# Kernel optimization log

Measured on AMD Instinct MI355X. Metric: run time of the kernel, lower is better.

The kernel has to match this reference:

```python
import jax, jax.numpy as jnp
import numpy as np

N_FLOWS = 40
S, D = 2048, 16384  # samples, latent dim n*q (n=8192, q=2)


def setup_inputs() -> dict:
    key = jax.random.key(0)
    kx, kw, ku, kb = jax.random.split(key, 4)
    X = jax.random.normal(kx, (S, D), dtype=jnp.float32)
    # Learned planar-flow parameters, stacked over the 40 layers.
    ws = jax.random.normal(kw, (N_FLOWS, D), dtype=jnp.float32) * 0.01
    us = jax.random.normal(ku, (N_FLOWS, D), dtype=jnp.float32) * 0.01
    bs = jax.random.normal(kb, (N_FLOWS,), dtype=jnp.float32) * 0.01
    return {"X": X, "ws": ws, "us": us, "bs": bs}


def _planar_chain(X, ws, us, bs):
    def step(x, params):
        w, u, b = params  # w,u: [D], b: scalar
        wu = jnp.dot(w, u)
        # invertibility constraint: m(a) = -1 + softplus(a)
        u_hat = u + ((-1.0 + jax.nn.softplus(wu)) - wu) * w / jnp.dot(w, w)
        act = jnp.tanh(x @ w + b)            # [S]
        return x + act[:, None] * u_hat, None  # rank-1 update

    X, _ = jax.lax.scan(step, X, (ws, us, bs))
    return X


def reference(X, ws, us, bs):
    return _planar_chain(X, ws, us, bs)
```

## Files before the change

### kernel.cpp

```cpp
#include <hip/hip_runtime.h>
#include <math.h>

#define D      16384
#define D4     4096
#define S      2048
#define NF     40
#define NFP    48
#define ROWS   8
#define TPB    1024
#define CH4    256
#define CHUNK  1024
#define NCHUNK 16
#define KSPLIT 8

#define WW_OFF     0
#define UW_OFF     1600
#define COEF_OFF   3200
#define AT_OFF     4096
#define WB_OFF     (AT_OFF + NF * S)
#define C0P_OFF    (WB_OFF + (NFP * D) / 2)
#define WS_NEED    (C0P_OFF + S * KSPLIT * NF)

typedef __attribute__((ext_vector_type(8))) __bf16 bf16x8;
typedef __attribute__((ext_vector_type(4))) float  f32x4;
union FragU { unsigned u[4]; bf16x8 b; };

__device__ __forceinline__ float dot4(float4 a, float4 b) {
    return fmaf(a.x, b.x, fmaf(a.y, b.y, fmaf(a.z, b.z, a.w * b.w)));
}
__device__ __forceinline__ void fma4(float4& o, float a, float4 u) {
    o.x = fmaf(a, u.x, o.x); o.y = fmaf(a, u.y, o.y);
    o.z = fmaf(a, u.z, o.z); o.w = fmaf(a, u.w, o.w);
}
__device__ __forceinline__ unsigned bpack(float lo, float hi) {
    unsigned a = __float_as_uint(lo);
    unsigned b = __float_as_uint(hi);
    a += 0x7fffu + ((a >> 16) & 1u);
    b += 0x7fffu + ((b >> 16) & 1u);
    return (a >> 16) | (b & 0xffff0000u);
}

__global__ __launch_bounds__(512) void pair_wb_kernel(const float* __restrict__ Wg,
                                                      const float* __restrict__ Ug,
                                                      float* __restrict__ tbl) {
    const int k = blockIdx.x >> 3;
    const int h = blockIdx.x & 7;
    const int t = threadIdx.x;
    uint2* Wb2 = (uint2*)((unsigned*)(tbl + WB_OFF) + (size_t)k * (D / 2));

    if (k >= NF) {
        Wb2[h * 512 + t] = make_uint2(0u, 0u);
        return;
    }

    const int j0 = h * 5;
    const int wave = t >> 6, lane = t & 63;
    const float4* W4 = (const float4*)Wg;
    const float4* U4 = (const float4*)Ug;

    float ww[5], wu[5], wkk = 0.f, wku = 0.f;
    float4 wkSave;
    #pragma unroll
    for (int j = 0; j < 5; ++j) { ww[j] = 0.f; wu[j] = 0.f; }

    for (int i = 0; i < 8; ++i) {
        const int pos = i * 512 + t;
        float4 wk = W4[(size_t)k * D4 + pos];
        float4 uk = U4[(size_t)k * D4 + pos];
        if (i == h) wkSave = wk;
        wkk += dot4(wk, wk);
        wku += dot4(wk, uk);
        #pragma unroll
        for (int j = 0; j < 5; ++j) {
            float4 wj = W4[(size_t)(j0 + j) * D4 + pos];
            float4 uj = U4[(size_t)(j0 + j) * D4 + pos];
            ww[j] += dot4(wk, wj);
            wu[j] += dot4(wk, uj);
        }
    }

    {
        uint2 p;
        p.x = bpack(wkSave.x, wkSave.y);
        p.y = bpack(wkSave.z, wkSave.w);
        Wb2[h * 512 + t] = p;
    }

    float v[12];
    #pragma unroll
    for (int j = 0; j < 5; ++j) { v[j] = ww[j]; v[5 + j] = wu[j]; }
    v[10] = wkk; v[11] = wku;
    #pragma unroll
    for (int e = 0; e < 12; ++e) {
        #pragma unroll
        for (int off = 32; off >= 1; off >>= 1) v[e] += __shfl_xor(v[e], off);
    }

    __shared__ float red[8][12];
    __shared__ float fin[12];
    if (lane == 0) {
        #pragma unroll
        for (int e = 0; e < 12; ++e) red[wave][e] = v[e];
    }
    __syncthreads();
    if (t < 12) {
        float s = 0.f;
        #pragma unroll
        for (int w = 0; w < 8; ++w) s += red[w][t];
        fin[t] = s;
        if (t < 5)       tbl[WW_OFF + k * NF + j0 + t] = s;
        else if (t < 10) tbl[UW_OFF + k * NF + j0 + (t - 5)] = s;
    }
    __syncthreads();
    if (t == 0 && h == 0) {
        float wwd = fin[10], wud = fin[11];
        float sp = (wud > 0.f) ? (wud + log1pf(expf(-wud))) : log1pf(expf(wud));
        tbl[COEF_OFF + k] = ((-1.f + sp) - wud) / wwd;
    }
}

__global__ __launch_bounds__(256) void gemm_part_kernel(const float* __restrict__ Xg,
                                                        float* __restrict__ tbl) {
    const int t = threadIdx.x, w = t >> 6, l = t & 63;
    const int rt = blockIdx.x >> 3, ks = blockIdx.x & 7;
    const int r = l & 15, kg = l >> 4;

    __shared__ float red[4][16][NFP + 1];

    const unsigned* WbU = (const unsigned*)(tbl + WB_OFF);
    f32x4 acc0 = {0.f, 0.f, 0.f, 0.f};
    f32x4 acc1 = acc0, acc2 = acc0;

    const float*    xrow = Xg + (size_t)(rt * 16 + r) * D + kg * 8;
    const unsigned* b0p = WbU + (size_t)(r)      * (D / 2) + kg * 4;
    const unsigned* b1p = WbU + (size_t)(16 + r) * (D / 2) + kg * 4;
    const unsigned* b2p = WbU + (size_t)(32 + r) * (D / 2) + kg * 4;
    const int kbase = ks * 2048 + w * 512;

    #pragma unroll 4
    for (int kk = 0; kk < 512; kk += 32) {
        const int kb = kbase + kk;
        float4 xa = *(const float4*)(xrow + kb);
        float4 xb = *(const float4*)(xrow + kb + 4);
        FragU af;
        af.u[0] = bpack(xa.x, xa.y); af.u[1] = bpack(xa.z, xa.w);
        af.u[2] = bpack(xb.x, xb.y); af.u[3] = bpack(xb.z, xb.w);
        const int ku = kb >> 1;
        bf16x8 b0 = *(const bf16x8*)(b0p + ku);
        bf16x8 b1 = *(const bf16x8*)(b1p + ku);
        bf16x8 b2 = *(const bf16x8*)(b2p + ku);
        acc0 = __builtin_amdgcn_mfma_f32_16x16x32_bf16(af.b, b0, acc0, 0, 0, 0);
        acc1 = __builtin_amdgcn_mfma_f32_16x16x32_bf16(af.b, b1, acc1, 0, 0, 0);
        acc2 = __builtin_amdgcn_mfma_f32_16x16x32_bf16(af.b, b2, acc2, 0, 0, 0);
    }

    #pragma unroll
    for (int q = 0; q < 4; ++q) {
        red[w][kg * 4 + q][r]      = acc0[q];
        red[w][kg * 4 + q][16 + r] = acc1[q];
        red[w][kg * 4 + q][32 + r] = acc2[q];
    }
    __syncthreads();

    float* c0p = tbl + C0P_OFF;
    for (int e = t; e < 16 * NF; e += 256) {
        const int row = e / NF, fl = e - row * NF;
        float s = red[0][row][fl] + red[1][row][fl] +
                  red[2][row][fl] + red[3][row][fl];
        c0p[((size_t)(rt * 16 + row) * KSPLIT + ks) * NF + fl] = s;
    }
}

__global__ __launch_bounds__(1024) void reduce_rec_kernel(const float* __restrict__ Bg,
                                                          float* __restrict__ tbl) {
    const int t = threadIdx.x;
    const int wave = t >> 6, lane = t & 63;

    __shared__ float gts[NF][NF + 1];
    __shared__ float bsS[NF];
    for (int e = t; e < NF * NF; e += 1024) {
        const int jj = e % NF;
        gts[e / NF][jj] = tbl[UW_OFF + e] + tbl[COEF_OFF + jj] * tbl[WW_OFF + e];
    }
    if (t < NF) bsS[t] = Bg[t];
    __syncthreads();

    const int g = blockIdx.x * 16 + wave;
    const float* cp = tbl + C0P_OFF + (size_t)g * (KSPLIT * NF);

    float c0 = 0.f;
    if (lane < NF) {
        #pragma unroll
        for (int s = 0; s < KSPLIT; ++s) c0 += cp[s * NF + lane];
        c0 += bsS[lane];
    }

    float aj = 0.f;
    for (int k = 0; k < NF; ++k) {
        float gv = (lane < k) ? gts[k][lane] : 0.f;
        float tv = aj * gv;
        #pragma unroll
        for (int off = 32; off >= 1; off >>= 1) tv += __shfl_xor(tv, off);
        float ck = __shfl(c0, k);
        float ak = tanhf(ck + tv);
        if (lane == k) aj = ak;
    }
    if (lane < NF) tbl[AT_OFF + (size_t)lane * S + g] = aj;
}

__global__ __launch_bounds__(256) void apply_kernel(const float* __restrict__ Xg,
                                                    const float* __restrict__ Wg,
                                                    const float* __restrict__ Ug,
                                                    const float* __restrict__ tbl,
                                                    float* __restrict__ Og) {
    const int bid = blockIdx.x;
    const int rblk = bid >> 3, cq = bid & 7;
    const int t = threadIdx.x;
    const int r0 = rblk * 8;

    const float4* X4 = (const float4*)Xg;
    const float4* W4 = (const float4*)Wg;
    const float4* U4 = (const float4*)Ug;
    const float*  aT = tbl + AT_OFF;
    float4* O4 = (float4*)Og;

    #pragma unroll 1
    for (int p = 0; p < 2; ++p) {
        const int col = cq * 512 + p * 256 + t;
        float4 o[8];
        #pragma unroll
        for (int r = 0; r < 8; ++r)
            o[r] = X4[(size_t)(r0 + r) * D4 + col];

        #pragma unroll 2
        for (int k = 0; k < NF; ++k) {
            float4 wv = W4[(size_t)k * D4 + col];
            float4 uu = U4[(size_t)k * D4 + col];
            const float cf = tbl[COEF_OFF + k];
            float4 uh;
            uh.x = fmaf(cf, wv.x, uu.x);
            uh.y = fmaf(cf, wv.y, uu.y);
            uh.z = fmaf(cf, wv.z, uu.z);
            uh.w = fmaf(cf, wv.w, uu.w);
            const float* ap = aT + (size_t)k * S + r0;
            fma4(o[0], ap[0], uh); fma4(o[1], ap[1], uh);
            fma4(o[2], ap[2], uh); fma4(o[3], ap[3], uh);
            fma4(o[4], ap[4], uh); fma4(o[5], ap[5], uh);
            fma4(o[6], ap[6], uh); fma4(o[7], ap[7], uh);
        }
        #pragma unroll
        for (int r = 0; r < 8; ++r)
            O4[(size_t)(r0 + r) * D4 + col] = o[r];
    }
}

__global__ __launch_bounds__(TPB) void flow_main_fb(const float* __restrict__ Xg,
                                                    const float* __restrict__ Wg,
                                                    const float* __restrict__ Ug,
                                                    const float* __restrict__ Bg,
                                                    const float* __restrict__ tbl,
                                                    float* __restrict__ Og) {
    const int t = threadIdx.x;
    const int wave = t >> 6, lane = t & 63;
    const int rowBase = blockIdx.x * ROWS;

    __shared__ __align__(16) float xs[2][ROWS][CHUNK];
    __shared__ __align__(16) float gts[NF][NF + 1];
    __shared__ __align__(16) float c0p[NF][ROWS];
    __shared__ __align__(16) float aTs[NF][ROWS];
    __shared__ float bsS[NF];
    __shared__ float coefS[NF];

    const float4* X4 = (const float4*)Xg;
    const float4* W4 = (const float4*)Wg;
    const float4* U4 = (const float4*)Ug;

    for (int e = t; e < NF * NF; e += TPB) {
        const int jj = e % NF;
        gts[e / NF][jj] = tbl[UW_OFF + e] + tbl[COEF_OFF + jj] * tbl[WW_OFF + e];
    }
    if (t < NF) { bsS[t] = Bg[t]; coefS[t] = tbl[COEF_OFF + t]; }

    const int srow = (t >> 8) * 2;
    const int sc4  = t & 255;

    float4 p0 = X4[(size_t)(rowBase + srow)     * D4 + sc4];
    float4 p1 = X4[(size_t)(rowBase + srow + 1) * D4 + sc4];
    *(float4*)&xs[0][srow][sc4 * 4]     = p0;
    *(float4*)&xs[0][srow + 1][sc4 * 4] = p1;
    __syncthreads();

    const int kt = wave & 7, rt = wave >> 3;
    const int k0 = kt * 5, r0 = rt * 4;

    float acc[4][5];
    #pragma unroll
    for (int r = 0; r < 4; ++r)
        #pragma unroll
        for (int kk = 0; kk < 5; ++kk) acc[r][kk] = 0.f;

    int b = 0;
    for (int c = 0; c < NCHUNK; ++c) {
        if (c + 1 < NCHUNK) {
            p0 = X4[(size_t)(rowBase + srow)     * D4 + (c + 1) * CH4 + sc4];
            p1 = X4[(size_t)(rowBase + srow + 1) * D4 + (c + 1) * CH4 + sc4];
        }
        #pragma unroll 1
        for (int s = 0; s < 4; ++s) {
            const int col4 = c * CH4 + s * 64 + lane;
            float4 wv[5];
            #pragma unroll
            for (int kk = 0; kk < 5; ++kk)
                wv[kk] = W4[(size_t)(k0 + kk) * D4 + col4];
            const int lc = (s * 64 + lane) * 4;
            #pragma unroll
            for (int r = 0; r < 4; ++r) {
                float4 xv = *(const float4*)&xs[b][r0 + r][lc];
                #pragma unroll
                for (int kk = 0; kk < 5; ++kk)
                    acc[r][kk] = fmaf(xv.x, wv[kk].x,
                                 fmaf(xv.y, wv[kk].y,
                                 fmaf(xv.z, wv[kk].z,
                                 fmaf(xv.w, wv[kk].w, acc[r][kk]))));
            }
        }
        if (c + 1 < NCHUNK) {
            *(float4*)&xs[b ^ 1][srow][sc4 * 4]     = p0;
            *(float4*)&xs[b ^ 1][srow + 1][sc4 * 4] = p1;
        }
        __syncthreads();
        b ^= 1;
    }

    #pragma unroll
    for (int r = 0; r < 4; ++r)
        #pragma unroll
        for (int kk = 0; kk < 5; ++kk) {
            float v = acc[r][kk];
            #pragma unroll
            for (int off = 32; off >= 1; off >>= 1) v += __shfl_xor(v, off);
            acc[r][kk] = v;
        }
    if (lane == 0) {
        #pragma unroll
        for (int kk = 0; kk < 5; ++kk)
            #pragma unroll
            for (int r = 0; r < 4; ++r)
                c0p[k0 + kk][r0 + r] = acc[r][kk];
    }
    __syncthreads();

    float4 o[ROWS];
    {
        const int col = wave * 64 + lane;
        #pragma unroll
        for (int r = 0; r < ROWS; ++r)
            o[r] = X4[(size_t)(rowBase + r) * D4 + col];
    }

    if (wave < ROWS) {
        const int r = wave, j = lane;
        float aj = 0.f;
        for (int k = 0; k < NF; ++k) {
            float gv = (j < k) ? gts[k][j] : 0.f;
            float tv = aj * gv;
            #pragma unroll
            for (int off = 32; off >= 1; off >>= 1) tv += __shfl_xor(tv, off);
            float sum = c0p[k][r] + bsS[k] + tv;
            float ak = tanhf(sum);
            if (j == k) aj = ak;
        }
        if (j < NF) aTs[j][r] = aj;
    }
    __syncthreads();

    float4* O4 = (float4*)Og;
    #pragma unroll 1
    for (int p = 0; p < 4; ++p) {
        const int col = p * 1024 + wave * 64 + lane;
        if (p > 0) {
            #pragma unroll
            for (int r = 0; r < ROWS; ++r)
                o[r] = X4[(size_t)(rowBase + r) * D4 + col];
        }
        #pragma unroll 2
        for (int k = 0; k < NF; ++k) {
            float4 uu = U4[(size_t)k * D4 + col];
            float4 wv = W4[(size_t)k * D4 + col];
            const float cf = coefS[k];
            float4 uh;
            uh.x = fmaf(cf, wv.x, uu.x);
            uh.y = fmaf(cf, wv.y, uu.y);
            uh.z = fmaf(cf, wv.z, uu.z);
            uh.w = fmaf(cf, wv.w, uu.w);
            float4 alo = *(const float4*)&aTs[k][0];
            float4 ahi = *(const float4*)&aTs[k][4];
            fma4(o[0], alo.x, uh); fma4(o[1], alo.y, uh);
            fma4(o[2], alo.z, uh); fma4(o[3], alo.w, uh);
            fma4(o[4], ahi.x, uh); fma4(o[5], ahi.y, uh);
            fma4(o[6], ahi.z, uh); fma4(o[7], ahi.w, uh);
        }
        #pragma unroll
        for (int r = 0; r < ROWS; ++r)
            O4[(size_t)(rowBase + r) * D4 + col] = o[r];
    }
}

extern "C" void kernel_launch(void* const* d_in, const int* in_sizes, int n_in,
                              void* d_out, int out_size, void* d_ws, size_t ws_size,
                              hipStream_t stream) {
    const float* X  = (const float*)d_in[0];
    const float* Wg = (const float*)d_in[1];
    const float* Ug = (const float*)d_in[2];
    const float* Bg = (const float*)d_in[3];
    float* out = (float*)d_out;
    float* tbl = (float*)d_ws;

    const bool fast = ws_size >= (size_t)WS_NEED * sizeof(float);

    if (fast) {
        pair_wb_kernel<<<NFP * 8, 512, 0, stream>>>(Wg, Ug, tbl);
        gemm_part_kernel<<<(S / 16) * KSPLIT, 256, 0, stream>>>(X, tbl);
        reduce_rec_kernel<<<S / 16, 1024, 0, stream>>>(Bg, tbl);
        apply_kernel<<<(S / 8) * 8, 256, 0, stream>>>(X, Wg, Ug, tbl, out);
    } else {
        pair_wb_kernel<<<NF * 8, 512, 0, stream>>>(Wg, Ug, tbl);
        flow_main_fb<<<S / ROWS, TPB, 0, stream>>>(X, Wg, Ug, Bg, tbl, out);
    }
}
```

Baseline: 142.9 us.

## Precompute u_hat once and stage activations in LDS for apply kernel

Adds a small kernel that materializes u_hat = u + coef*w for all flows into workspace, so the apply kernel reads one vector per flow instead of two plus a coefficient. The activation table is transposed to row-major [S][NF], and each apply block loads its 8x40 slice into shared memory, reading it as float4 instead of scattered scalar global loads. This cuts per-block global traffic and scalar loads in the hot loop, at the cost of an extra launch and a u_hat write/read pass (about 2.6MB). The fallback path skips the bf16 W pack.

```diff
diff --git a/kernel.cpp b/kernel.cpp
--- a/kernel.cpp
+++ b/kernel.cpp
@@ -19,6 +19,7 @@
 #define AT_OFF     4096
 #define WB_OFF     (AT_OFF + NF * S)
 #define C0P_OFF    (WB_OFF + (NFP * D) / 2)
+#define UH_OFF     C0P_OFF
 #define WS_NEED    (C0P_OFF + S * KSPLIT * NF)
 
 typedef __attribute__((ext_vector_type(8))) __bf16 bf16x8;
@@ -42,7 +43,8 @@
 
 __global__ __launch_bounds__(512) void pair_wb_kernel(const float* __restrict__ Wg,
                                                       const float* __restrict__ Ug,
-                                                      float* __restrict__ tbl) {
+                                                      float* __restrict__ tbl,
+                                                      int doWb) {
     const int k = blockIdx.x >> 3;
     const int h = blockIdx.x & 7;
     const int t = threadIdx.x;
@@ -79,7 +81,7 @@
         }
     }
 
-    {
+    if (doWb) {
         uint2 p;
         p.x = bpack(wkSave.x, wkSave.y);
         p.y = bpack(wkSave.z, wkSave.w);
@@ -205,12 +207,25 @@
         float ak = tanhf(ck + tv);
         if (lane == k) aj = ak;
     }
-    if (lane < NF) tbl[AT_OFF + (size_t)lane * S + g] = aj;
+    if (lane < NF) tbl[AT_OFF + (size_t)g * NF + lane] = aj;
+}
+
+__global__ __launch_bounds__(256) void uh_kernel(const float* __restrict__ Wg,
+                                                 const float* __restrict__ Ug,
+                                                 float* __restrict__ tbl) {
+    const int k = blockIdx.x >> 4;
+    const int h = blockIdx.x & 15;
+    const float cf = tbl[COEF_OFF + k];
+    const int i = h * 256 + threadIdx.x;
+    const float4 w = ((const float4*)Wg)[(size_t)k * D4 + i];
+    const float4 u = ((const float4*)Ug)[(size_t)k * D4 + i];
+    float4 r;
+    r.x = fmaf(cf, w.x, u.x); r.y = fmaf(cf, w.y, u.y);
+    r.z = fmaf(cf, w.z, u.z); r.w = fmaf(cf, w.w, u.w);
+    ((float4*)(tbl + UH_OFF))[(size_t)k * D4 + i] = r;
 }
 
 __global__ __launch_bounds__(256) void apply_kernel(const float* __restrict__ Xg,
-                                                    const float* __restrict__ Wg,
-                                                    const float* __restrict__ Ug,
                                                     const float* __restrict__ tbl,
                                                     float* __restrict__ Og) {
     const int bid = blockIdx.x;
@@ -218,10 +233,15 @@
     const int t = threadIdx.x;
     const int r0 = rblk * 8;
 
-    const float4* X4 = (const float4*)Xg;
-    const float4* W4 = (const float4*)Wg;
-    const float4* U4 = (const float4*)Ug;
-    const float*  aT = tbl + AT_OFF;
+    __shared__ __align__(16) float aL[NF][8];
+    for (int e = t; e < NF * 8; e += 256) {
+        const int r = e / NF, k = e - r * NF;
+        aL[k][r] = tbl[AT_OFF + (size_t)(r0 + r) * NF + k];
+    }
+    __syncthreads();
+
+    const float4* X4  = (const float4*)Xg;
+    const float4* UH4 = (const float4*)(tbl + UH_OFF);
     float4* O4 = (float4*)Og;
 
     #pragma unroll 1
@@ -232,21 +252,15 @@
         for (int r = 0; r < 8; ++r)
             o[r] = X4[(size_t)(r0 + r) * D4 + col];
 
-        #pragma unroll 2
+        #pragma unroll 4
         for (int k = 0; k < NF; ++k) {
-            float4 wv = W4[(size_t)k * D4 + col];
-            float4 uu = U4[(size_t)k * D4 + col];
-            const float cf = tbl[COEF_OFF + k];
-            float4 uh;
-            uh.x = fmaf(cf, wv.x, uu.x);
-            uh.y = fmaf(cf, wv.y, uu.y);
-            uh.z = fmaf(cf, wv.z, uu.z);
-            uh.w = fmaf(cf, wv.w, uu.w);
-            const float* ap = aT + (size_t)k * S + r0;
-            fma4(o[0], ap[0], uh); fma4(o[1], ap[1], uh);
-            fma4(o[2], ap[2], uh); fma4(o[3], ap[3], uh);
-            fma4(o[4], ap[4], uh); fma4(o[5], ap[5], uh);
-            fma4(o[6], ap[6], uh); fma4(o[7], ap[7], uh);
+            float4 uh = UH4[(size_t)k * D4 + col];
+            float4 alo = *(const float4*)&aL[k][0];
+            float4 ahi = *(const float4*)&aL[k][4];
+            fma4(o[0], alo.x, uh); fma4(o[1], alo.y, uh);
+            fma4(o[2], alo.z, uh); fma4(o[3], alo.w, uh);
+            fma4(o[4], ahi.x, uh); fma4(o[5], ahi.y, uh);
+            fma4(o[6], ahi.z, uh); fma4(o[7], ahi.w, uh);
         }
         #pragma unroll
         for (int r = 0; r < 8; ++r)
@@ -419,12 +433,13 @@
     const bool fast = ws_size >= (size_t)WS_NEED * sizeof(float);
 
     if (fast) {
-        pair_wb_kernel<<<NFP * 8, 512, 0, stream>>>(Wg, Ug, tbl);
+        pair_wb_kernel<<<NFP * 8, 512, 0, stream>>>(Wg, Ug, tbl, 1);
         gemm_part_kernel<<<(S / 16) * KSPLIT, 256, 0, stream>>>(X, tbl);
         reduce_rec_kernel<<<S / 16, 1024, 0, stream>>>(Bg, tbl);
-        apply_kernel<<<(S / 8) * 8, 256, 0, stream>>>(X, Wg, Ug, tbl, out);
+        uh_kernel<<<NF * 16, 256, 0, stream>>>(Wg, Ug, tbl);
+        apply_kernel<<<(S / 8) * 8, 256, 0, stream>>>(X, tbl, out);
     } else {
-        pair_wb_kernel<<<NF * 8, 512, 0, stream>>>(Wg, Ug, tbl);
+        pair_wb_kernel<<<NF * 8, 512, 0, stream>>>(Wg, Ug, tbl, 0);
         flow_main_fb<<<S / ROWS, TPB, 0, stream>>>(X, Wg, Ug, Bg, tbl, out);
     }
 }
```

After: 129.8 us. 1.1x faster.
